# Optimization experiments

Measured on AMD Instinct MI355X. Metric: run time of the kernel, lower is better.

The kernel has to match this reference:

```python
import jax, jax.numpy as jnp
import numpy as np
from math import sqrt

EPS = 1e-5
N_BISECT = 30

def _entmax15_impl(x):
    # alpha=1.5 entmax along last axis via bisection (entmax_bisect, alpha=1.5)
    xs = x * 0.5  # (alpha-1) * x
    mx = jnp.max(xs, axis=-1, keepdims=True)
    d = xs.shape[-1]
    lo = mx - 1.0
    hi = mx - d ** -0.5  # d^{-(alpha-1)}
    def body(i, carry):
        lo, hi = carry
        mid = 0.5 * (lo + hi)
        f = jnp.sum(jnp.square(jnp.maximum(xs - mid, 0.0)), -1, keepdims=True) - 1.0
        lo = jnp.where(f > 0, mid, lo)
        hi = jnp.where(f > 0, hi, mid)
        return lo, hi
    lo, hi = jax.lax.fori_loop(0, N_BISECT, body, (lo, hi))
    tau = 0.5 * (lo + hi)
    p = jnp.square(jnp.maximum(xs - tau, 0.0))
    return p / jnp.sum(p, -1, keepdims=True)

@jax.custom_vjp
def entmax15(x):
    return _entmax15_impl(x)

def _entmax15_fwd(x):
    p = _entmax15_impl(x)
    return p, p

def _entmax15_bwd(p, g):
    # exact entmax-1.5 backward (entmax repo): gppr = sqrt(p) on support
    s = jnp.sqrt(p)
    dx = g * s
    q = jnp.sum(dx, -1, keepdims=True) / jnp.sum(s, -1, keepdims=True)
    return (dx - q * s,)

entmax15.defvjp(_entmax15_fwd, _entmax15_bwd)

def layer_norm(x, g, b):
    m = jnp.mean(x, -1, keepdims=True)
    v = jnp.var(x, -1, keepdims=True)
    return (x - m) / jnp.sqrt(v + EPS) * g + b

def mlp(x, w1, b1, w2, b2):
    return jax.nn.gelu(x @ w1 + b1, approximate=False) @ w2 + b2

def hopfield_core(q_in, k_in, H, wq, bq, wk, bk, wv, bv, wo, bo):
    # Faithful to Hopfield.forward with mix=True; `values` arg of the torch
    # module is ignored (it recomputes value_projection(key_projection(keys))).
    B, L, _ = q_in.shape
    S = k_in.shape[1]
    q = (q_in @ wq + bq).reshape(B, L, H, -1)
    k = k_in @ wk + bk
    v = (k @ wv + bv).reshape(B, S, H, -1)
    kh = k.reshape(B, S, H, -1)
    E = q.shape[-1]
    scores = jnp.einsum('blhe,bshe->bhls', q, kh) * (1.0 / sqrt(E))
    A = entmax15(scores)
    out = jnp.einsum('bhls,bshd->blhd', A, v)
    # mix=True: transpose(2,1) then view(B, L, -1) on contiguous (B,H,L,D)
    out = jnp.transpose(out, (0, 2, 1, 3)).reshape(B, L, -1)
    return out @ wo + bo

def _forward(n_heads, x, ct_wq, ct_bq, ct_wk, ct_bk, ct_wv, ct_bv, ct_wo, ct_bo,
             cs_wq, cs_bq, cs_wk, cs_bk, cs_wv, cs_bv, cs_wo, cs_bo, cs_key,
             hp_wq, hp_bq, hp_wk, hp_bk, hp_wv, hp_bv, hp_wo, hp_bo,
             n1_g, n1_b, n2_g, n2_b, n3_g, n3_b, n4_g, n4_b,
             m1_w1, m1_b1, m1_w2, m1_b2, m2_w1, m2_b1, m2_w2, m2_b2):
    b, ts_d, seg, d = x.shape
    time_in = x.reshape(b * ts_d, seg, d)
    time_enc = hopfield_core(time_in, time_in, n_heads,
                             ct_wq, ct_bq, ct_wk, ct_bk, ct_wv, ct_bv, ct_wo, ct_bo)
    dim_in = layer_norm(time_in + time_enc, n1_g, n1_b)
    dim_in = layer_norm(dim_in + mlp(dim_in, m1_w1, m1_b1, m1_w2, m1_b2), n2_g, n2_b)
    # '(b ts_d) seg d -> (b seg) ts_d d'
    series_in = dim_in.reshape(b, ts_d, seg, d).transpose(0, 2, 1, 3).reshape(b * seg, ts_d, d)
    # HopfieldPooling: learned stored patterns as keys
    pooled_keys = jnp.broadcast_to(cs_key, (b * seg,) + cs_key.shape[1:])
    series_h = hopfield_core(series_in, pooled_keys, n_heads,
                             cs_wq, cs_bq, cs_wk, cs_bk, cs_wv, cs_bv, cs_wo, cs_bo)
    pooled_h = hopfield_core(series_in, series_in, n_heads,
                             hp_wq, hp_bq, hp_wk, hp_bk, hp_wv, hp_bv, hp_wo, hp_bo)
    dim_enc = layer_norm(series_h + pooled_h, n3_g, n3_b)
    dim_enc = layer_norm(dim_enc + mlp(dim_enc, m2_w1, m2_b1, m2_w2, m2_b2), n4_g, n4_b)
    # '(b seg) ts_d d -> b ts_d seg d'
    return dim_enc.reshape(b, seg, ts_d, d).transpose(0, 2, 1, 3)

def setup_inputs() -> dict:
    b, ts_d, seg, d, h, dff, factor = 8, 32, 64, 1024, 16, 4096, 10
    keys = iter(jax.random.split(jax.random.key(0), 64))
    def rn(shape, s=0.02):
        return jax.random.normal(next(keys), shape, jnp.float32) * s
    inp = {"x": jax.random.normal(next(keys), (b, ts_d, seg, d), jnp.float32)}
    for p in ("ct", "cs", "hp"):
        inp[p + "_wq"] = rn((d, d)); inp[p + "_bq"] = rn((d,))
        inp[p + "_wk"] = rn((d, d)); inp[p + "_bk"] = rn((d,))
        inp[p + "_wv"] = rn((d, d)); inp[p + "_bv"] = rn((d,))
        inp[p + "_wo"] = rn((d, d)); inp[p + "_bo"] = rn((d,))
    inp["cs_key"] = rn((1, factor, d), 0.1)
    for i in ("1", "2", "3", "4"):
        inp["n" + i + "_g"] = jnp.ones((d,), jnp.float32)
        inp["n" + i + "_b"] = jnp.zeros((d,), jnp.float32)
    for m in ("m1", "m2"):
        inp[m + "_w1"] = rn((d, dff)); inp[m + "_b1"] = rn((dff,))
        inp[m + "_w2"] = rn((dff, d)); inp[m + "_b2"] = rn((d,))
    inp["n_heads"] = h
    return inp

def reference(x, ct_wq, ct_bq, ct_wk, ct_bk, ct_wv, ct_bv, ct_wo, ct_bo,
              cs_wq, cs_bq, cs_wk, cs_bk, cs_wv, cs_bv, cs_wo, cs_bo, cs_key,
              hp_wq, hp_bq, hp_wk, hp_bk, hp_wv, hp_bv, hp_wo, hp_bo,
              n1_g, n1_b, n2_g, n2_b, n3_g, n3_b, n4_g, n4_b,
              m1_w1, m1_b1, m1_w2, m1_b2, m2_w1, m2_b1, m2_w2, m2_b2, n_heads):
    return _forward(n_heads, x, ct_wq, ct_bq, ct_wk, ct_bk, ct_wv, ct_bv, ct_wo, ct_bo,
                    cs_wq, cs_bq, cs_wk, cs_bk, cs_wv, cs_bv, cs_wo, cs_bo, cs_key,
                    hp_wq, hp_bq, hp_wk, hp_bk, hp_wv, hp_bv, hp_wo, hp_bo,
                    n1_g, n1_b, n2_g, n2_b, n3_g, n3_b, n4_g, n4_b,
                    m1_w1, m1_b1, m1_w2, m1_b2, m2_w1, m2_b1, m2_w2, m2_b2)
```

## Files before the change

### kernel.cpp

```cpp
#include <hip/hip_runtime.h>
#include <cstdio>

typedef __bf16 bf16x8 __attribute__((ext_vector_type(8)));
typedef float f32x4 __attribute__((ext_vector_type(4)));
typedef int i32x4 __attribute__((ext_vector_type(4)));
typedef unsigned short u16x4 __attribute__((ext_vector_type(4)));

__device__ __forceinline__ float bf2f(unsigned short u) {
  union { unsigned int i; float f; } x; x.i = ((unsigned int)u) << 16; return x.f;
}
__device__ __forceinline__ unsigned short f2bf(float f) {
  union { float f; unsigned int i; } x; x.f = f;
  unsigned int r = x.i + 0x7fffu + ((x.i >> 16) & 1u);
  return (unsigned short)(r >> 16);
}

__device__ __forceinline__ void gl2lds16(const unsigned short* g, unsigned short* l) {
  __builtin_amdgcn_global_load_lds((const __attribute__((address_space(1))) unsigned int*)g,
                                   (__attribute__((address_space(3))) unsigned int*)l, 16, 0, 0);
}

__global__ __launch_bounds__(256) void k_cast(const float* __restrict__ in,
                                              unsigned short* __restrict__ out, int n4) {
  int i = blockIdx.x * 256 + threadIdx.x;
  if (i >= n4) return;
  f32x4 v = ((const f32x4*)in)[i];
  u16x4 o;
  o[0] = f2bf(v[0]); o[1] = f2bf(v[1]); o[2] = f2bf(v[2]); o[3] = f2bf(v[3]);
  ((u16x4*)out)[i] = o;
}

__global__ __launch_bounds__(256) void k_tcast(const float* __restrict__ src,
                                               unsigned short* __restrict__ dst,
                                               int K, int N) {
  __shared__ float tile[32][33];
  int gx = blockIdx.x * 32;
  int gy = blockIdx.y * 32;
  int t = threadIdx.x;
  int c = t & 31, r0 = t >> 5;
#pragma unroll
  for (int i = 0; i < 4; i++) {
    int r = r0 + i * 8;
    tile[r][c] = src[(size_t)(gy + r) * N + gx + c];
  }
  __syncthreads();
#pragma unroll
  for (int i = 0; i < 4; i++) {
    int r = r0 + i * 8;
    dst[(size_t)(gx + r) * K + gy + c] = f2bf(tile[c][r]);
  }
}

__global__ __launch_bounds__(256) void k_bfold(const float* __restrict__ bk,
                                               const float* __restrict__ wv,
                                               const float* __restrict__ bv,
                                               float* __restrict__ out) {
  int n = blockIdx.x * 256 + threadIdx.x;
  float acc = bv[n];
#pragma unroll 8
  for (int j = 0; j < 1024; j++) acc += bk[j] * wv[(size_t)j * 1024 + n];
  out[n] = acc;
}

__global__ __launch_bounds__(256) void k_cpb(const float* __restrict__ a,
                                             const float* __restrict__ b,
                                             float* __restrict__ out) {
  int t = blockIdx.x * 256 + threadIdx.x;
  out[t] = a[t];
  out[1024 + t] = b[t];
}

template <bool GELU>
__global__ __launch_bounds__(512, 2) void k_gemm8(const unsigned short* __restrict__ A,
                                                  const unsigned short* __restrict__ Bt,
                                                  const float* __restrict__ bias,
                                                  unsigned short* __restrict__ C,
                                                  int M, int N, int K) {
  __shared__ unsigned short As[2][256 * 64];
  __shared__ unsigned short Bs[2][256 * 64];
  const int rowA0 = blockIdx.y * 256, colB0 = blockIdx.x * 256;
  const int t = threadIdx.x, w = t >> 6, lane = t & 63;
  const int wm = w >> 2, wn = w & 3;
  const int g = lane >> 4, ra = lane & 15;
  const int koff0 = (((0 * 4 + g) ^ (ra & 7)) * 8);
  const int koff1 = (((1 * 4 + g) ^ (ra & 7)) * 8);
  const int srow = w * 8 + (lane >> 3);
  const int schunk = ((lane & 7) ^ ((lane >> 3) & 7)) * 8;

  f32x4 acc[8][4] = {};

  auto stageA = [&](int buf, int kk) {
#pragma unroll
    for (int gq = 0; gq < 4; gq++)
      gl2lds16(A + (size_t)(rowA0 + gq * 64 + srow) * K + kk + schunk,
               &As[buf][gq * 4096 + w * 512]);
  };
  auto stageB = [&](int buf, int kk) {
#pragma unroll
    for (int gq = 0; gq < 4; gq++)
      gl2lds16(Bt + (size_t)(colB0 + gq * 64 + srow) * K + kk + schunk,
               &Bs[buf][gq * 4096 + w * 512]);
  };

  const int NT = K >> 6;
  stageA(0, 0); stageB(0, 0);
  asm volatile("s_waitcnt vmcnt(0)" ::: "memory");
  __builtin_amdgcn_sched_barrier(0);
  __builtin_amdgcn_s_barrier();

  bf16x8 aH[4][2], bH[2][2][2];
  const int arow0 = wm * 128, brow0 = wn * 64;
  for (int j = 0; j < NT; ++j) {
    const int buf = j & 1;
    const unsigned short* Ab = &As[buf][0];
    const unsigned short* Bb = &Bs[buf][0];
#pragma unroll
    for (int fr = 0; fr < 4; fr++) {
      aH[fr][0] = *(const bf16x8*)&Ab[(arow0 + fr * 16 + ra) * 64 + koff0];
      aH[fr][1] = *(const bf16x8*)&Ab[(arow0 + fr * 16 + ra) * 64 + koff1];
    }
#pragma unroll
    for (int fc = 0; fc < 2; fc++) {
      bH[0][fc][0] = *(const bf16x8*)&Bb[(brow0 + fc * 16 + ra) * 64 + koff0];
      bH[0][fc][1] = *(const bf16x8*)&Bb[(brow0 + fc * 16 + ra) * 64 + koff1];
    }
    if (j + 1 < NT) stageA(buf ^ 1, (j + 1) << 6);
    __builtin_amdgcn_sched_barrier(0);
    __builtin_amdgcn_s_barrier();
    __builtin_amdgcn_sched_barrier(0);
    __builtin_amdgcn_s_setprio(1);
#pragma unroll
    for (int fr = 0; fr < 4; fr++)
#pragma unroll
      for (int fc = 0; fc < 2; fc++)
#pragma unroll
        for (int ks = 0; ks < 2; ks++)
          acc[fr][fc] = __builtin_amdgcn_mfma_f32_16x16x32_bf16(aH[fr][ks], bH[0][fc][ks], acc[fr][fc], 0, 0, 0);
    __builtin_amdgcn_s_setprio(0);
    __builtin_amdgcn_sched_barrier(0);
    __builtin_amdgcn_s_barrier();
#pragma unroll
    for (int fc = 0; fc < 2; fc++) {
      bH[1][fc][0] = *(const bf16x8*)&Bb[(brow0 + 32 + fc * 16 + ra) * 64 + koff0];
      bH[1][fc][1] = *(const bf16x8*)&Bb[(brow0 + 32 + fc * 16 + ra) * 64 + koff1];
    }
    if (j + 1 < NT) stageB(buf ^ 1, (j + 1) << 6);
    __builtin_amdgcn_sched_barrier(0);
    __builtin_amdgcn_s_barrier();
    __builtin_amdgcn_sched_barrier(0);
    __builtin_amdgcn_s_setprio(1);
#pragma unroll
    for (int fr = 0; fr < 4; fr++)
#pragma unroll
      for (int fc = 0; fc < 2; fc++)
#pragma unroll
        for (int ks = 0; ks < 2; ks++)
          acc[fr][2 + fc] = __builtin_amdgcn_mfma_f32_16x16x32_bf16(aH[fr][ks], bH[1][fc][ks], acc[fr][2 + fc], 0, 0, 0);
    __builtin_amdgcn_s_setprio(0);
    __builtin_amdgcn_sched_barrier(0);
    __builtin_amdgcn_s_barrier();
#pragma unroll
    for (int fr = 0; fr < 4; fr++) {
      aH[fr][0] = *(const bf16x8*)&Ab[(arow0 + 64 + fr * 16 + ra) * 64 + koff0];
      aH[fr][1] = *(const bf16x8*)&Ab[(arow0 + 64 + fr * 16 + ra) * 64 + koff1];
    }
    __builtin_amdgcn_sched_barrier(0);
    __builtin_amdgcn_s_barrier();
    __builtin_amdgcn_sched_barrier(0);
    __builtin_amdgcn_s_setprio(1);
#pragma unroll
    for (int fr = 0; fr < 4; fr++)
#pragma unroll
      for (int fc = 0; fc < 2; fc++)
#pragma unroll
        for (int ks = 0; ks < 2; ks++)
          acc[4 + fr][fc] = __builtin_amdgcn_mfma_f32_16x16x32_bf16(aH[fr][ks], bH[0][fc][ks], acc[4 + fr][fc], 0, 0, 0);
    __builtin_amdgcn_s_setprio(0);
    __builtin_amdgcn_sched_barrier(0);
    __builtin_amdgcn_s_barrier();
    __builtin_amdgcn_s_setprio(1);
#pragma unroll
    for (int fr = 0; fr < 4; fr++)
#pragma unroll
      for (int fc = 0; fc < 2; fc++)
#pragma unroll
        for (int ks = 0; ks < 2; ks++)
          acc[4 + fr][2 + fc] = __builtin_amdgcn_mfma_f32_16x16x32_bf16(aH[fr][ks], bH[1][fc][ks], acc[4 + fr][2 + fc], 0, 0, 0);
    __builtin_amdgcn_s_setprio(0);
    if (j + 1 < NT) asm volatile("s_waitcnt vmcnt(0)" ::: "memory");
    __builtin_amdgcn_sched_barrier(0);
    __builtin_amdgcn_s_barrier();
  }

  unsigned short* Ep = &As[0][0] + w * 1024;
  const int grow0 = rowA0 + wm * 128;
  const int gcol0 = colB0 + wn * 64;
  float bv[4];
#pragma unroll
  for (int n = 0; n < 4; n++) bv[n] = bias ? bias[gcol0 + n * 16 + ra] : 0.f;
  const int rdrow = lane >> 3, rg = lane & 7;
#pragma unroll
  for (int m = 0; m < 8; m++) {
#pragma unroll
    for (int n = 0; n < 4; n++)
#pragma unroll
      for (int i = 0; i < 4; i++) {
        int r = g * 4 + i;
        float v = acc[m][n][i] + bv[n];
        if (GELU) v = 0.5f * v * (1.f + erff(v * 0.70710678118654752f));
        Ep[r * 64 + ((ra + n * 16) ^ ((r & 7) << 3))] = f2bf(v);
      }
    asm volatile("s_waitcnt lgkmcnt(0)" ::: "memory");
    __builtin_amdgcn_sched_barrier(0);
#pragma unroll
    for (int p = 0; p < 2; p++) {
      int rr = p * 8 + rdrow;
      bf16x8 val = *(const bf16x8*)&Ep[rr * 64 + ((rg ^ (rr & 7)) << 3)];
      *(bf16x8*)&C[(size_t)(grow0 + m * 16 + rr) * N + gcol0 + rg * 8] = val;
    }
    asm volatile("s_waitcnt lgkmcnt(0)" ::: "memory");
  }
}

__global__ __launch_bounds__(256) void k_gemmS(const unsigned short* __restrict__ A,
                                               const unsigned short* __restrict__ Bt,
                                               const float* __restrict__ bias,
                                               unsigned short* __restrict__ C,
                                               int M, int N, int K) {
  __shared__ unsigned short As[3][128 * 32];
  __shared__ unsigned short Bs[3][128 * 32];
  const int rowA0 = blockIdx.y * 128, colB0 = blockIdx.x * 128;
  const int t = threadIdx.x, w = t >> 6, lane = t & 63;
  const int wr = w >> 1, wc = w & 1;
  const int srow = w * 16 + (lane >> 2);
  const int schunk = (lane & 3) ^ ((lane >> 3) & 3);
  const unsigned short* pa = A + (size_t)(rowA0 + srow) * K + schunk * 8;
  const unsigned short* pb = Bt + (size_t)(colB0 + srow) * K + schunk * 8;
  const size_t row64 = (size_t)64 * K;
  f32x4 acc[4][4] = {};
  const int g = lane >> 4, ra = lane & 15;
  const int gp8 = (g ^ ((ra >> 1) & 3)) * 8;
  auto stage = [&](int buf, int kk) {
    gl2lds16(pa + kk, &As[buf][w * 512]);
    gl2lds16(pa + row64 + kk, &As[buf][2048 + w * 512]);
    gl2lds16(pb + kk, &Bs[buf][w * 512]);
    gl2lds16(pb + row64 + kk, &Bs[buf][2048 + w * 512]);
  };
  const int NT = K >> 5;
  stage(0, 0);
  if (NT > 1) stage(1, 32);
  int cur = 0;
  for (int j = 0; j < NT; ++j) {
    if (j + 1 < NT) asm volatile("s_waitcnt vmcnt(4)" ::: "memory");
    else            asm volatile("s_waitcnt vmcnt(0)" ::: "memory");
    __syncthreads();
    if (j + 2 < NT) { int nb = cur + 2; if (nb >= 3) nb -= 3; stage(nb, (j + 2) * 32); }
    bf16x8 af[4], bfr[4];
#pragma unroll
    for (int m = 0; m < 4; m++)
      af[m] = *(const bf16x8*)&As[cur][(wr * 64 + m * 16 + ra) * 32 + gp8];
#pragma unroll
    for (int n = 0; n < 4; n++)
      bfr[n] = *(const bf16x8*)&Bs[cur][(wc * 64 + n * 16 + ra) * 32 + gp8];
#pragma unroll
    for (int m = 0; m < 4; m++)
#pragma unroll
      for (int n = 0; n < 4; n++)
        acc[m][n] = __builtin_amdgcn_mfma_f32_16x16x32_bf16(af[m], bfr[n], acc[m][n], 0, 0, 0);
    __syncthreads();
    cur += 1; if (cur >= 3) cur -= 3;
  }
  const int cr = g * 4, cc = ra;
#pragma unroll
  for (int m = 0; m < 4; m++) {
    int grow = rowA0 + wr * 64 + m * 16 + cr;
#pragma unroll
    for (int n = 0; n < 4; n++) {
      int gcol = colB0 + wc * 64 + n * 16 + cc;
      float bvv = bias ? bias[gcol] : 0.f;
#pragma unroll
      for (int i = 0; i < 4; i++)
        C[(size_t)(grow + i) * N + gcol] = f2bf(acc[m][n][i] + bvv);
    }
  }
}

__global__ __launch_bounds__(256) void k_gemm10(const unsigned short* __restrict__ A,
                                                const unsigned short* __restrict__ Bt,
                                                const float* __restrict__ bias,
                                                unsigned short* __restrict__ C) {
  __shared__ float af[1024];
  int m = blockIdx.x, nb = blockIdx.y;
  int t = threadIdx.x;
#pragma unroll
  for (int i = 0; i < 4; i++) af[t * 4 + i] = bf2f(A[(size_t)m * 1024 + t * 4 + i]);
  __syncthreads();
  int w = t >> 6, lane = t & 63;
  for (int n = nb * 64 + w; n < nb * 64 + 64; n += 4) {
    const unsigned short* brow = Bt + (size_t)n * 1024 + lane * 16;
    float acc = 0.f;
#pragma unroll
    for (int j = 0; j < 16; j++) acc += af[lane * 16 + j] * bf2f(brow[j]);
#pragma unroll
    for (int o = 32; o; o >>= 1) acc += __shfl_xor(acc, o);
    if (lane == 0) C[(size_t)m * 1024 + n] = f2bf(acc + bias[n]);
  }
}

template <int L, int S, bool SHARED>
__global__ __launch_bounds__(256) void k_attn(const unsigned short* __restrict__ Q,
                                              const unsigned short* __restrict__ Kb,
                                              const unsigned short* __restrict__ Vb,
                                              unsigned short* __restrict__ Out, int RS) {
  constexpr int SP = (S <= 32) ? 32 : 64;
  constexpr int QST = 72;
  constexpr int VST = SP + 8;
  constexpr int CST = SP + 4;
  __shared__ unsigned short Qs[L * QST];
  __shared__ unsigned short Ks[SP * QST];
  __shared__ unsigned short Vt[64 * VST];
  __shared__ float Sc[L * CST];
  __shared__ float Rps[L];
  const int blk = blockIdx.x, batch = blk >> 4, h = blk & 15;
  const int t = threadIdx.x, w = t >> 6, lane = t & 63;
  for (int c = t; c < L * 8; c += 256) {
    int r = c >> 3, ch = (c & 7) * 8;
    *(i32x4*)&Qs[r * QST + ch] =
        *(const i32x4*)&Q[((size_t)(batch * L + r)) * RS + h * 64 + ch];
  }
  for (int c = t; c < SP * 8; c += 256) {
    int r = c >> 3, ch = (c & 7) * 8;
    i32x4 v = {0, 0, 0, 0};
    if (r < S) {
      size_t rb = SHARED ? (size_t)r : (size_t)(batch * S + r);
      v = *(const i32x4*)&Kb[rb * RS + h * 64 + ch];
    }
    *(i32x4*)&Ks[r * QST + ch] = v;
  }
  for (int c = t; c < SP * 64; c += 256) {
    int s = c >> 6, e = c & 63;
    unsigned short v = 0;
    if (s < S) {
      size_t rb = SHARED ? (size_t)s : (size_t)(batch * S + s);
      v = Vb[rb * RS + h * 64 + e];
    }
    Vt[e * VST + s] = v;
  }
  __syncthreads();
  const int ka = (lane >> 4) * 8, ra = lane & 15;
  const int cr = (lane >> 4) * 4, cc = lane & 15;
  constexpr int NT = SP / 16, TT = (L / 16) * NT;
  for (int tt = w; tt < TT; tt += 4) {
    int m = tt / NT, n = tt % NT;
    f32x4 a = {0.f, 0.f, 0.f, 0.f};
#pragma unroll
    for (int ks = 0; ks < 2; ks++) {
      bf16x8 af = *(const bf16x8*)&Qs[(m * 16 + ra) * QST + ks * 32 + ka];
      bf16x8 bf = *(const bf16x8*)&Ks[(n * 16 + ra) * QST + ks * 32 + ka];
      a = __builtin_amdgcn_mfma_f32_16x16x32_bf16(af, bf, a, 0, 0, 0);
    }
#pragma unroll
    for (int i = 0; i < 4; i++)
      Sc[(m * 16 + cr + i) * CST + n * 16 + cc] = a[i] * 0.0625f;
  }
  __syncthreads();
  constexpr int G = 256 / L, RW = 64 / G, SL = SP / G;
  const int row = w * RW + lane / G, sub = lane % G;
  float xs[SL];
#pragma unroll
  for (int j = 0; j < SL; j++) {
    int s = sub * SL + j;
    float v = Sc[row * CST + s];
    if (S < SP && s >= S) v = -1e30f;
    xs[j] = v;
  }
  float mx = xs[0];
#pragma unroll
  for (int j = 1; j < SL; j++) mx = fmaxf(mx, xs[j]);
#pragma unroll
  for (int o = G / 2; o; o >>= 1) mx = fmaxf(mx, __shfl_xor(mx, o));
  const float hoff = (S == 64) ? 0.125f : (S == 32) ? 0.17677669529663687f : 0.31622776601683794f;
  float lo = mx - 1.f, hi = mx - hoff;
#pragma unroll 1
  for (int it = 0; it < 26; it++) {
    float mid = 0.5f * (lo + hi);
    float f = 0.f;
#pragma unroll
    for (int j = 0; j < SL; j++) { float dd = fmaxf(xs[j] - mid, 0.f); f += dd * dd; }
#pragma unroll
    for (int o = G / 2; o; o >>= 1) f += __shfl_xor(f, o);
    bool gt = f > 1.f;
    lo = gt ? mid : lo;
    hi = gt ? hi : mid;
  }
  float tau = 0.5f * (lo + hi);
  float ps = 0.f;
#pragma unroll
  for (int j = 0; j < SL; j++) { float dd = fmaxf(xs[j] - tau, 0.f); xs[j] = dd * dd; ps += xs[j]; }
#pragma unroll
  for (int o = G / 2; o; o >>= 1) ps += __shfl_xor(ps, o);
  if (sub == 0) Rps[row] = 1.f / ps;
  unsigned short* Pb = Qs;
#pragma unroll
  for (int j = 0; j < SL; j += 4) {
    u16x4 pv;
#pragma unroll
    for (int jj = 0; jj < 4; jj++) pv[jj] = f2bf(xs[j + jj]);
    *(u16x4*)&Pb[row * VST + sub * SL + j] = pv;
  }
  __syncthreads();
  constexpr int TT2 = (L / 16) * 4;
  for (int tt = w; tt < TT2; tt += 4) {
    int m = tt >> 2, n = tt & 3;
    f32x4 a = {0.f, 0.f, 0.f, 0.f};
#pragma unroll
    for (int ks = 0; ks < SP / 32; ks++) {
      bf16x8 af = *(const bf16x8*)&Pb[(m * 16 + ra) * VST + ks * 32 + ka];
      bf16x8 bf = *(const bf16x8*)&Vt[(n * 16 + ra) * VST + ks * 32 + ka];
      a = __builtin_amdgcn_mfma_f32_16x16x32_bf16(af, bf, a, 0, 0, 0);
    }
#pragma unroll
    for (int i = 0; i < 4; i++) {
      int l = m * 16 + cr + i, e = n * 16 + cc;
      float val = a[i] * Rps[l];
      int l_new = h * (L / 16) + (l >> 4);
      int cg = (l & 15) * 64 + e;
      Out[((size_t)(batch * L + l_new)) * 1024 + cg] = f2bf(val);
    }
  }
}

template <int MODE, bool F32OUT>
__global__ __launch_bounds__(256) void k_ln(const unsigned short* __restrict__ a,
                                            const unsigned short* __restrict__ b,
                                            const float* __restrict__ g,
                                            const float* __restrict__ be,
                                            void* __restrict__ outp) {
  __shared__ float red[8];
  int r = blockIdx.x, t = threadIdx.x;
  size_t base = (size_t)r * 1024 + t * 4;
  u16x4 av = *(const u16x4*)(a + base);
  u16x4 bv = *(const u16x4*)(b + base);
  float x[4];
  float s = 0.f, ss = 0.f;
#pragma unroll
  for (int i = 0; i < 4; i++) {
    x[i] = bf2f(av[i]) + bf2f(bv[i]);
    s += x[i]; ss += x[i] * x[i];
  }
#pragma unroll
  for (int o = 32; o; o >>= 1) { s += __shfl_xor(s, o); ss += __shfl_xor(ss, o); }
  int w = t >> 6;
  if ((t & 63) == 0) { red[w] = s; red[4 + w] = ss; }
  __syncthreads();
  s = red[0] + red[1] + red[2] + red[3];
  ss = red[4] + red[5] + red[6] + red[7];
  float mean = s * (1.f / 1024.f);
  float var = ss * (1.f / 1024.f) - mean * mean;
  float rstd = rsqrtf(var + 1e-5f);
  int orow;
  if (MODE == 0) orow = r;
  else if (MODE == 1) { int bi = r >> 11, rem = r & 2047; int tt = rem >> 6, sd = rem & 63; orow = (bi << 11) + sd * 32 + tt; }
  else { int bi = r >> 11, rem = r & 2047; int sd = rem >> 5, tt = rem & 31; orow = (bi << 11) + tt * 64 + sd; }
  size_t ob = (size_t)orow * 1024 + t * 4;
  if (F32OUT) {
    f32x4 y;
#pragma unroll
    for (int i = 0; i < 4; i++) y[i] = (x[i] - mean) * rstd * g[t * 4 + i] + be[t * 4 + i];
    *(f32x4*)((float*)outp + ob) = y;
  } else {
    u16x4 y;
#pragma unroll
    for (int i = 0; i < 4; i++) y[i] = f2bf((x[i] - mean) * rstd * g[t * 4 + i] + be[t * 4 + i]);
    *(u16x4*)((unsigned short*)outp + ob) = y;
  }
}


extern "C" void kernel_launch(void* const* d_in, const int* in_sizes, int n_in,
                              void* d_out, int out_size, void* d_ws, size_t ws_size,
                              hipStream_t stream) {
  const int M = 16384;
  if (n_in < 43 || in_sizes[0] != 16777216 || in_sizes[25] != 10240 || in_sizes[34] != 4194304) {
    fprintf(stderr, "kernel_launch: unexpected input layout (n_in=%d)\n", n_in);
    return;
  }
  const float* x = (const float*)d_in[0];
  const float* w[3][4]; const float* bia[3][4];
  for (int p = 0; p < 3; p++) {
    w[p][0] = (const float*)d_in[1 + 8 * p + 0]; bia[p][0] = (const float*)d_in[1 + 8 * p + 1];
    w[p][1] = (const float*)d_in[1 + 8 * p + 2]; bia[p][1] = (const float*)d_in[1 + 8 * p + 3];
    w[p][2] = (const float*)d_in[1 + 8 * p + 4]; bia[p][2] = (const float*)d_in[1 + 8 * p + 5];
    w[p][3] = (const float*)d_in[1 + 8 * p + 6]; bia[p][3] = (const float*)d_in[1 + 8 * p + 7];
  }
  const float* cs_key = (const float*)d_in[25];
  const float* ng[4]; const float* nb[4];
  for (int i = 0; i < 4; i++) { ng[i] = (const float*)d_in[26 + 2 * i]; nb[i] = (const float*)d_in[27 + 2 * i]; }
  const float* m_w1[2]; const float* m_b1[2]; const float* m_w2[2]; const float* m_b2[2];
  for (int i = 0; i < 2; i++) {
    m_w1[i] = (const float*)d_in[34 + 4 * i]; m_b1[i] = (const float*)d_in[35 + 4 * i];
    m_w2[i] = (const float*)d_in[36 + 4 * i]; m_b2[i] = (const float*)d_in[37 + 4 * i];
  }

  char* base = (char*)d_ws; size_t off = 0;
  auto alloc = [&](size_t bytes) -> void* {
    off = (off + 255) & ~(size_t)255;
    void* p = base + off; off += bytes; return p;
  };
  const size_t W1M = (size_t)1024 * 1024;
  unsigned short* W3ct = (unsigned short*)alloc(3 * W1M * 2);
  unsigned short* W3hp = (unsigned short*)alloc(3 * W1M * 2);
  unsigned short* Woct = (unsigned short*)alloc(W1M * 2);
  unsigned short* Wohp = (unsigned short*)alloc(W1M * 2);
  unsigned short* Wocs = (unsigned short*)alloc(W1M * 2);
  unsigned short* Wqcs = (unsigned short*)alloc(W1M * 2);
  unsigned short* Wkcs = (unsigned short*)alloc(W1M * 2);
  unsigned short* Wvcs = (unsigned short*)alloc(W1M * 2);
  unsigned short* Wm1u = (unsigned short*)alloc((size_t)4096 * 1024 * 2);
  unsigned short* Wm1d = (unsigned short*)alloc((size_t)1024 * 4096 * 2);
  unsigned short* Wm2u = (unsigned short*)alloc((size_t)4096 * 1024 * 2);
  unsigned short* Wm2d = (unsigned short*)alloc((size_t)1024 * 4096 * 2);
  float* b3ct = (float*)alloc(3072 * 4);
  float* b3hp = (float*)alloc(3072 * 4);
  unsigned short* KeyB = (unsigned short*)alloc((size_t)10 * 1024 * 2);
  unsigned short* Kcs = (unsigned short*)alloc((size_t)10 * 1024 * 2);
  unsigned short* Vcs = (unsigned short*)alloc((size_t)10 * 1024 * 2);
  unsigned short* S[6];
  for (int i = 0; i < 6; i++) S[i] = (unsigned short*)alloc((size_t)M * 1024 * 2);
  if (off > ws_size) {
    fprintf(stderr, "kernel_launch: ws too small: need %zu have %zu\n", off, ws_size);
    return;
  }
  unsigned short* Wvt_ct = S[1];
  unsigned short* Wraw_ct = S[1] + W1M;
  unsigned short* Wvt_hp = S[1] + 2 * W1M;
  unsigned short* Wraw_hp = S[1] + 3 * W1M;

  auto gemm = [&](const unsigned short* Ap, const unsigned short* Bt, const float* bi,
                  unsigned short* Cp, int Mm, int Nn, int Kk, bool gelu) {
    dim3 gg(Nn / 256, Mm / 256);
    if (gelu) k_gemm8<true><<<gg, 512, 0, stream>>>(Ap, Bt, bi, Cp, Mm, Nn, Kk);
    else      k_gemm8<false><<<gg, 512, 0, stream>>>(Ap, Bt, bi, Cp, Mm, Nn, Kk);
  };
  auto tc = [&](const float* src, unsigned short* dst) {
    k_tcast<<<dim3(32, 32), 256, 0, stream>>>(src, dst, 1024, 1024);
  };

  tc(w[0][0], W3ct); tc(w[0][1], W3ct + W1M);
  tc(w[2][0], W3hp); tc(w[2][1], W3hp + W1M);
  tc(w[0][3], Woct); tc(w[2][3], Wohp); tc(w[1][3], Wocs);
  tc(w[1][0], Wqcs); tc(w[1][1], Wkcs); tc(w[1][2], Wvcs);
  k_tcast<<<dim3(128, 32), 256, 0, stream>>>(m_w1[0], Wm1u, 1024, 4096);
  k_tcast<<<dim3(32, 128), 256, 0, stream>>>(m_w2[0], Wm1d, 4096, 1024);
  k_tcast<<<dim3(128, 32), 256, 0, stream>>>(m_w1[1], Wm2u, 1024, 4096);
  k_tcast<<<dim3(32, 128), 256, 0, stream>>>(m_w2[1], Wm2d, 4096, 1024);
  tc(w[0][2], Wvt_ct); k_cast<<<1024, 256, 0, stream>>>(w[0][1], Wraw_ct, 262144);
  tc(w[2][2], Wvt_hp); k_cast<<<1024, 256, 0, stream>>>(w[2][1], Wraw_hp, 262144);
  k_cast<<<16384, 256, 0, stream>>>(x, S[0], 16777216 / 4);
  k_cast<<<10, 256, 0, stream>>>(cs_key, KeyB, 10240 / 4);
  k_gemmS<<<dim3(8, 8), 256, 0, stream>>>(Wvt_ct, Wraw_ct, nullptr, W3ct + 2 * W1M, 1024, 1024, 1024);
  k_gemmS<<<dim3(8, 8), 256, 0, stream>>>(Wvt_hp, Wraw_hp, nullptr, W3hp + 2 * W1M, 1024, 1024, 1024);
  k_cpb<<<4, 256, 0, stream>>>(bia[0][0], bia[0][1], b3ct);
  k_bfold<<<4, 256, 0, stream>>>(bia[0][1], w[0][2], bia[0][2], b3ct + 2048);
  k_cpb<<<4, 256, 0, stream>>>(bia[2][0], bia[2][1], b3hp);
  k_bfold<<<4, 256, 0, stream>>>(bia[2][1], w[2][2], bia[2][2], b3hp + 2048);
  k_gemm10<<<dim3(10, 16), 256, 0, stream>>>(KeyB, Wkcs, bia[1][1], Kcs);
  k_gemm10<<<dim3(10, 16), 256, 0, stream>>>(Kcs, Wvcs, bia[1][2], Vcs);

  gemm(S[0], W3ct, b3ct, S[1], M, 3072, 1024, false);
  k_attn<64, 64, false><<<256 * 16, 256, 0, stream>>>(S[1], S[1] + 1024, S[1] + 2048, S[4], 3072);
  gemm(S[4], Woct, bia[0][3], S[5], M, 1024, 1024, false);
  k_ln<0, false><<<M, 256, 0, stream>>>(S[0], S[5], ng[0], nb[0], S[1]);
  gemm(S[1], Wm1u, m_b1[0], S[2], M, 4096, 1024, true);
  gemm(S[2], Wm1d, m_b2[0], S[0], M, 1024, 4096, false);
  k_ln<1, false><<<M, 256, 0, stream>>>(S[1], S[0], ng[1], nb[1], S[2]);

  gemm(S[2], W3hp, b3hp, S[3], M, 3072, 1024, false);
  k_attn<32, 32, false><<<512 * 16, 256, 0, stream>>>(S[3], S[3] + 1024, S[3] + 2048, S[0], 3072);
  gemm(S[0], Wohp, bia[2][3], S[1], M, 1024, 1024, false);
  gemm(S[2], Wqcs, bia[1][0], S[3], M, 1024, 1024, false);
  k_attn<32, 10, true><<<512 * 16, 256, 0, stream>>>(S[3], Kcs, Vcs, S[4], 1024);
  gemm(S[4], Wocs, bia[1][3], S[5], M, 1024, 1024, false);
  k_ln<0, false><<<M, 256, 0, stream>>>(S[5], S[1], ng[2], nb[2], S[0]);
  gemm(S[0], Wm2u, m_b1[1], S[1], M, 4096, 1024, true);
  gemm(S[1], Wm2d, m_b2[1], S[5], M, 1024, 4096, false);
  k_ln<2, true><<<M, 256, 0, stream>>>(S[0], S[5], ng[3], nb[3], d_out);
}
```

Baseline: 1.671 ms.

## Fold cross-attention query projection into keys and simplify GEMM pipeline

Precomputes Wq·K^T per head so the 10-key cross-attention scores come straight from a skinny GEMM against the normed activations. That removes the full 1024x1024 query projection. A dedicated per-row entmax kernel over 10 keys and a small PV-mix kernel replace the generic attention kernel. The main GEMM is rewritten with K-tile 32 and a simple double-buffered loop instead of the hand-scheduled 64-K pipeline, with a 128-row tile variant used for N=1024 GEMMs to raise block count. The risks are reduced precision (bf16 rounding of the folded weights), 26 bisection steps instead of 30, and losing the tuned scheduling in the big GEMMs.

```diff
diff --git a/kernel.cpp b/kernel.cpp
--- a/kernel.cpp
+++ b/kernel.cpp
@@ -70,137 +70,165 @@
   out[1024 + t] = b[t];
 }
 
-template <bool GELU>
-__global__ __launch_bounds__(512, 2) void k_gemm8(const unsigned short* __restrict__ A,
-                                                  const unsigned short* __restrict__ Bt,
-                                                  const float* __restrict__ bias,
-                                                  unsigned short* __restrict__ C,
-                                                  int M, int N, int K) {
-  __shared__ unsigned short As[2][256 * 64];
-  __shared__ unsigned short Bs[2][256 * 64];
-  const int rowA0 = blockIdx.y * 256, colB0 = blockIdx.x * 256;
+__global__ __launch_bounds__(256) void k_wqk(const unsigned short* __restrict__ wqT,
+                                             const float* __restrict__ bq,
+                                             const unsigned short* __restrict__ Kcs,
+                                             unsigned short* __restrict__ BtQK,
+                                             float* __restrict__ bqk) {
+  int n = blockIdx.x, h = n >> 4, s = n & 15, t = threadIdx.x;
+  if (s >= 10) {
+    ((u16x4*)(BtQK + (size_t)n * 1024))[t] = u16x4{0, 0, 0, 0};
+    if (t == 0) bqk[n] = 0.f;
+    return;
+  }
+  float acc[4] = {0.f, 0.f, 0.f, 0.f};
+  for (int e = 0; e < 64; e++) {
+    float kv = bf2f(Kcs[s * 1024 + h * 64 + e]);
+    u16x4 rv = ((const u16x4*)(wqT + (size_t)(h * 64 + e) * 1024))[t];
+#pragma unroll
+    for (int i = 0; i < 4; i++) acc[i] += bf2f(rv[i]) * kv;
+  }
+  u16x4 o;
+#pragma unroll
+  for (int i = 0; i < 4; i++) o[i] = f2bf(acc[i]);
+  ((u16x4*)(BtQK + (size_t)n * 1024))[t] = o;
+  if (t == 0) {
+    float b = 0.f;
+    for (int e = 0; e < 64; e++) b += bq[h * 64 + e] * bf2f(Kcs[s * 1024 + h * 64 + e]);
+    bqk[n] = b;
+  }
+}
+
+__global__ __launch_bounds__(256) void k_entmax10(const unsigned short* __restrict__ SC,
+                                                  unsigned short* __restrict__ A) {
+  int t = threadIdx.x;
+  int m = blockIdx.x * 16 + (t >> 4), h = t & 15;
+  const unsigned short* p = SC + (size_t)m * 256 + h * 16;
+  float xs[10], mx = -1e30f;
+#pragma unroll
+  for (int s = 0; s < 10; s++) { xs[s] = bf2f(p[s]) * 0.0625f; mx = fmaxf(mx, xs[s]); }
+  float lo = mx - 1.f, hi = mx - 0.31622776601683794f;
+#pragma unroll 1
+  for (int it = 0; it < 26; it++) {
+    float mid = 0.5f * (lo + hi);
+    float f = 0.f;
+#pragma unroll
+    for (int s = 0; s < 10; s++) { float dd = fmaxf(xs[s] - mid, 0.f); f += dd * dd; }
+    bool gt = f > 1.f;
+    lo = gt ? mid : lo;
+    hi = gt ? hi : mid;
+  }
+  float tau = 0.5f * (lo + hi), ps = 0.f;
+#pragma unroll
+  for (int s = 0; s < 10; s++) { float dd = fmaxf(xs[s] - tau, 0.f); xs[s] = dd * dd; ps += xs[s]; }
+  float r = 1.f / ps;
+  unsigned short* q = A + (size_t)m * 256 + h * 16;
+  u16x4 o0, o1, o2, o3;
+#pragma unroll
+  for (int i = 0; i < 4; i++) o0[i] = f2bf(xs[i] * r);
+#pragma unroll
+  for (int i = 0; i < 4; i++) o1[i] = f2bf(xs[4 + i] * r);
+  o2[0] = f2bf(xs[8] * r); o2[1] = f2bf(xs[9] * r); o2[2] = 0; o2[3] = 0;
+  o3[0] = o3[1] = o3[2] = o3[3] = 0;
+  ((u16x4*)q)[0] = o0; ((u16x4*)q)[1] = o1; ((u16x4*)q)[2] = o2; ((u16x4*)q)[3] = o3;
+}
+
+__global__ __launch_bounds__(256) void k_pvmix(const unsigned short* __restrict__ A,
+                                               const unsigned short* __restrict__ Vcs,
+                                               unsigned short* __restrict__ Out) {
+  __shared__ float Vs[10][64];
+  __shared__ float Asm[16][10];
+  const int row = blockIdx.x;
+  const int b = row >> 5, ln = row & 31;
+  const int h = ln >> 1, lbase = (ln & 1) * 16;
+  const int t = threadIdx.x;
+  if (t < 160) {
+    int j = t / 10, s = t - j * 10;
+    Asm[j][s] = bf2f(A[((size_t)(b * 32 + lbase + j)) * 256 + h * 16 + s]);
+  }
+  for (int idx = t; idx < 640; idx += 256) {
+    int s = idx >> 6, d = idx & 63;
+    Vs[s][d] = bf2f(Vcs[s * 1024 + h * 64 + d]);
+  }
+  __syncthreads();
+  const int j = t >> 4, d0 = (t & 15) * 4;
+  float acc[4] = {0.f, 0.f, 0.f, 0.f};
+#pragma unroll
+  for (int s = 0; s < 10; s++) {
+    float a = Asm[j][s];
+#pragma unroll
+    for (int i = 0; i < 4; i++) acc[i] += a * Vs[s][d0 + i];
+  }
+  u16x4 o;
+#pragma unroll
+  for (int i = 0; i < 4; i++) o[i] = f2bf(acc[i]);
+  ((u16x4*)(Out + (size_t)row * 1024))[t] = o;
+}
+
+template <int BM, bool GELU>
+__global__ __launch_bounds__(512, 4) void k_gemm(const unsigned short* __restrict__ A,
+                                                 const unsigned short* __restrict__ Bt,
+                                                 const float* __restrict__ bias,
+                                                 unsigned short* __restrict__ C,
+                                                 int M, int N, int K) {
+  constexpr int RPW = BM / 2;
+  constexpr int RF = RPW / 16;
+  __shared__ unsigned short As[2][BM * 32];
+  __shared__ unsigned short Bs[2][256 * 32];
+  const int rowA0 = blockIdx.y * BM, colB0 = blockIdx.x * 256;
   const int t = threadIdx.x, w = t >> 6, lane = t & 63;
   const int wm = w >> 2, wn = w & 3;
   const int g = lane >> 4, ra = lane & 15;
-  const int koff0 = (((0 * 4 + g) ^ (ra & 7)) * 8);
-  const int koff1 = (((1 * 4 + g) ^ (ra & 7)) * 8);
-  const int srow = w * 8 + (lane >> 3);
-  const int schunk = ((lane & 7) ^ ((lane >> 3) & 7)) * 8;
-
-  f32x4 acc[8][4] = {};
-
-  auto stageA = [&](int buf, int kk) {
-#pragma unroll
-    for (int gq = 0; gq < 4; gq++)
-      gl2lds16(A + (size_t)(rowA0 + gq * 64 + srow) * K + kk + schunk,
-               &As[buf][gq * 4096 + w * 512]);
+  const int gp8 = (g ^ ((ra >> 1) & 3)) * 8;
+  const int srow = lane >> 2;
+  const int schunk = ((lane & 3) ^ ((lane >> 3) & 3)) * 8;
+
+  f32x4 acc[RF][4] = {};
+
+  auto stage = [&](int buf, int kk) {
+#pragma unroll
+    for (int i = 0; i < BM / 128; i++)
+      gl2lds16(A + (size_t)(rowA0 + w * 16 + i * 128 + srow) * K + kk + schunk,
+               &As[buf][(w * 16 + i * 128) * 32]);
+#pragma unroll
+    for (int i = 0; i < 2; i++)
+      gl2lds16(Bt + (size_t)(colB0 + w * 16 + i * 128 + srow) * K + kk + schunk,
+               &Bs[buf][(w * 16 + i * 128) * 32]);
   };
-  auto stageB = [&](int buf, int kk) {
-#pragma unroll
-    for (int gq = 0; gq < 4; gq++)
-      gl2lds16(Bt + (size_t)(colB0 + gq * 64 + srow) * K + kk + schunk,
-               &Bs[buf][gq * 4096 + w * 512]);
-  };
-
-  const int NT = K >> 6;
-  stageA(0, 0); stageB(0, 0);
-  asm volatile("s_waitcnt vmcnt(0)" ::: "memory");
-  __builtin_amdgcn_sched_barrier(0);
-  __builtin_amdgcn_s_barrier();
-
-  bf16x8 aH[4][2], bH[2][2][2];
-  const int arow0 = wm * 128, brow0 = wn * 64;
+
+  const int NT = K >> 5;
+  stage(0, 0);
+  int buf = 0;
   for (int j = 0; j < NT; ++j) {
-    const int buf = j & 1;
+    asm volatile("s_waitcnt vmcnt(0)" ::: "memory");
+    __syncthreads();
+    if (j + 1 < NT) stage(buf ^ 1, (j + 1) * 32);
     const unsigned short* Ab = &As[buf][0];
     const unsigned short* Bb = &Bs[buf][0];
-#pragma unroll
-    for (int fr = 0; fr < 4; fr++) {
-      aH[fr][0] = *(const bf16x8*)&Ab[(arow0 + fr * 16 + ra) * 64 + koff0];
-      aH[fr][1] = *(const bf16x8*)&Ab[(arow0 + fr * 16 + ra) * 64 + koff1];
-    }
-#pragma unroll
-    for (int fc = 0; fc < 2; fc++) {
-      bH[0][fc][0] = *(const bf16x8*)&Bb[(brow0 + fc * 16 + ra) * 64 + koff0];
-      bH[0][fc][1] = *(const bf16x8*)&Bb[(brow0 + fc * 16 + ra) * 64 + koff1];
-    }
-    if (j + 1 < NT) stageA(buf ^ 1, (j + 1) << 6);
-    __builtin_amdgcn_sched_barrier(0);
-    __builtin_amdgcn_s_barrier();
-    __builtin_amdgcn_sched_barrier(0);
-    __builtin_amdgcn_s_setprio(1);
-#pragma unroll
-    for (int fr = 0; fr < 4; fr++)
-#pragma unroll
-      for (int fc = 0; fc < 2; fc++)
-#pragma unroll
-        for (int ks = 0; ks < 2; ks++)
-          acc[fr][fc] = __builtin_amdgcn_mfma_f32_16x16x32_bf16(aH[fr][ks], bH[0][fc][ks], acc[fr][fc], 0, 0, 0);
-    __builtin_amdgcn_s_setprio(0);
-    __builtin_amdgcn_sched_barrier(0);
-    __builtin_amdgcn_s_barrier();
-#pragma unroll
-    for (int fc = 0; fc < 2; fc++) {
-      bH[1][fc][0] = *(const bf16x8*)&Bb[(brow0 + 32 + fc * 16 + ra) * 64 + koff0];
-      bH[1][fc][1] = *(const bf16x8*)&Bb[(brow0 + 32 + fc * 16 + ra) * 64 + koff1];
-    }
-    if (j + 1 < NT) stageB(buf ^ 1, (j + 1) << 6);
-    __builtin_amdgcn_sched_barrier(0);
-    __builtin_amdgcn_s_barrier();
-    __builtin_amdgcn_sched_barrier(0);
-    __builtin_amdgcn_s_setprio(1);
-#pragma unroll
-    for (int fr = 0; fr < 4; fr++)
-#pragma unroll
-      for (int fc = 0; fc < 2; fc++)
-#pragma unroll
-        for (int ks = 0; ks < 2; ks++)
-          acc[fr][2 + fc] = __builtin_amdgcn_mfma_f32_16x16x32_bf16(aH[fr][ks], bH[1][fc][ks], acc[fr][2 + fc], 0, 0, 0);
-    __builtin_amdgcn_s_setprio(0);
-    __builtin_amdgcn_sched_barrier(0);
-    __builtin_amdgcn_s_barrier();
-#pragma unroll
-    for (int fr = 0; fr < 4; fr++) {
-      aH[fr][0] = *(const bf16x8*)&Ab[(arow0 + 64 + fr * 16 + ra) * 64 + koff0];
-      aH[fr][1] = *(const bf16x8*)&Ab[(arow0 + 64 + fr * 16 + ra) * 64 + koff1];
-    }
-    __builtin_amdgcn_sched_barrier(0);
-    __builtin_amdgcn_s_barrier();
-    __builtin_amdgcn_sched_barrier(0);
-    __builtin_amdgcn_s_setprio(1);
-#pragma unroll
-    for (int fr = 0; fr < 4; fr++)
-#pragma unroll
-      for (int fc = 0; fc < 2; fc++)
-#pragma unroll
-        for (int ks = 0; ks < 2; ks++)
-          acc[4 + fr][fc] = __builtin_amdgcn_mfma_f32_16x16x32_bf16(aH[fr][ks], bH[0][fc][ks], acc[4 + fr][fc], 0, 0, 0);
-    __builtin_amdgcn_s_setprio(0);
-    __builtin_amdgcn_sched_barrier(0);
-    __builtin_amdgcn_s_barrier();
-    __builtin_amdgcn_s_setprio(1);
-#pragma unroll
-    for (int fr = 0; fr < 4; fr++)
-#pragma unroll
-      for (int fc = 0; fc < 2; fc++)
-#pragma unroll
-        for (int ks = 0; ks < 2; ks++)
-          acc[4 + fr][2 + fc] = __builtin_amdgcn_mfma_f32_16x16x32_bf16(aH[fr][ks], bH[1][fc][ks], acc[4 + fr][2 + fc], 0, 0, 0);
-    __builtin_amdgcn_s_setprio(0);
-    if (j + 1 < NT) asm volatile("s_waitcnt vmcnt(0)" ::: "memory");
-    __builtin_amdgcn_sched_barrier(0);
-    __builtin_amdgcn_s_barrier();
-  }
+    bf16x8 bfr[4];
+#pragma unroll
+    for (int fc = 0; fc < 4; fc++)
+      bfr[fc] = *(const bf16x8*)&Bb[(wn * 64 + fc * 16 + ra) * 32 + gp8];
+#pragma unroll
+    for (int fr = 0; fr < RF; fr++) {
+      bf16x8 af = *(const bf16x8*)&Ab[(wm * RPW + fr * 16 + ra) * 32 + gp8];
+#pragma unroll
+      for (int fc = 0; fc < 4; fc++)
+        acc[fr][fc] = __builtin_amdgcn_mfma_f32_16x16x32_bf16(af, bfr[fc], acc[fr][fc], 0, 0, 0);
+    }
+    buf ^= 1;
+  }
+  __syncthreads();
 
   unsigned short* Ep = &As[0][0] + w * 1024;
-  const int grow0 = rowA0 + wm * 128;
+  const int grow0 = rowA0 + wm * RPW;
   const int gcol0 = colB0 + wn * 64;
   float bv[4];
 #pragma unroll
   for (int n = 0; n < 4; n++) bv[n] = bias ? bias[gcol0 + n * 16 + ra] : 0.f;
   const int rdrow = lane >> 3, rg = lane & 7;
 #pragma unroll
-  for (int m = 0; m < 8; m++) {
+  for (int m = 0; m < RF; m++) {
 #pragma unroll
     for (int n = 0; n < 4; n++)
 #pragma unroll
@@ -520,6 +548,8 @@
   unsigned short* Wm1d = (unsigned short*)alloc((size_t)1024 * 4096 * 2);
   unsigned short* Wm2u = (unsigned short*)alloc((size_t)4096 * 1024 * 2);
   unsigned short* Wm2d = (unsigned short*)alloc((size_t)1024 * 4096 * 2);
+  unsigned short* BtQK = (unsigned short*)alloc((size_t)256 * 1024 * 2);
+  float* bqk = (float*)alloc(256 * 4);
   float* b3ct = (float*)alloc(3072 * 4);
   float* b3hp = (float*)alloc(3072 * 4);
   unsigned short* KeyB = (unsigned short*)alloc((size_t)10 * 1024 * 2);
@@ -537,10 +567,16 @@
   unsigned short* Wraw_hp = S[1] + 3 * W1M;
 
   auto gemm = [&](const unsigned short* Ap, const unsigned short* Bt, const float* bi,
-                  unsigned short* Cp, int Mm, int Nn, int Kk, bool gelu) {
-    dim3 gg(Nn / 256, Mm / 256);
-    if (gelu) k_gemm8<true><<<gg, 512, 0, stream>>>(Ap, Bt, bi, Cp, Mm, Nn, Kk);
-    else      k_gemm8<false><<<gg, 512, 0, stream>>>(Ap, Bt, bi, Cp, Mm, Nn, Kk);
+                  unsigned short* Cp, int Mm, int Nn, int Kk, bool gelu, bool bm128) {
+    if (bm128) {
+      dim3 gg(Nn / 256, Mm / 128);
+      if (gelu) k_gemm<128, true><<<gg, 512, 0, stream>>>(Ap, Bt, bi, Cp, Mm, Nn, Kk);
+      else      k_gemm<128, false><<<gg, 512, 0, stream>>>(Ap, Bt, bi, Cp, Mm, Nn, Kk);
+    } else {
+      dim3 gg(Nn / 256, Mm / 256);
+      if (gelu) k_gemm<256, true><<<gg, 512, 0, stream>>>(Ap, Bt, bi, Cp, Mm, Nn, Kk);
+      else      k_gemm<256, false><<<gg, 512, 0, stream>>>(Ap, Bt, bi, Cp, Mm, Nn, Kk);
+    }
   };
   auto tc = [&](const float* src, unsigned short* dst) {
     k_tcast<<<dim3(32, 32), 256, 0, stream>>>(src, dst, 1024, 1024);
@@ -566,23 +602,25 @@
   k_bfold<<<4, 256, 0, stream>>>(bia[2][1], w[2][2], bia[2][2], b3hp + 2048);
   k_gemm10<<<dim3(10, 16), 256, 0, stream>>>(KeyB, Wkcs, bia[1][1], Kcs);
   k_gemm10<<<dim3(10, 16), 256, 0, stream>>>(Kcs, Wvcs, bia[1][2], Vcs);
-
-  gemm(S[0], W3ct, b3ct, S[1], M, 3072, 1024, false);
+  k_wqk<<<256, 256, 0, stream>>>(Wqcs, bia[1][0], Kcs, BtQK, bqk);
+
+  gemm(S[0], W3ct, b3ct, S[1], M, 3072, 1024, false, false);
   k_attn<64, 64, false><<<256 * 16, 256, 0, stream>>>(S[1], S[1] + 1024, S[1] + 2048, S[4], 3072);
-  gemm(S[4], Woct, bia[0][3], S[5], M, 1024, 1024, false);
+  gemm(S[4], Woct, bia[0][3], S[5], M, 1024, 1024, false, true);
   k_ln<0, false><<<M, 256, 0, stream>>>(S[0], S[5], ng[0], nb[0], S[1]);
-  gemm(S[1], Wm1u, m_b1[0], S[2], M, 4096, 1024, true);
-  gemm(S[2], Wm1d, m_b2[0], S[0], M, 1024, 4096, false);
+  gemm(S[1], Wm1u, m_b1[0], S[2], M, 4096, 1024, true, false);
+  gemm(S[2], Wm1d, m_b2[0], S[0], M, 1024, 4096, false, true);
   k_ln<1, false><<<M, 256, 0, stream>>>(S[1], S[0], ng[1], nb[1], S[2]);
 
-  gemm(S[2], W3hp, b3hp, S[3], M, 3072, 1024, false);
+  gemm(S[2], W3hp, b3hp, S[3], M, 3072, 1024, false, false);
   k_attn<32, 32, false><<<512 * 16, 256, 0, stream>>>(S[3], S[3] + 1024, S[3] + 2048, S[0], 3072);
-  gemm(S[0], Wohp, bia[2][3], S[1], M, 1024, 1024, false);
-  gemm(S[2], Wqcs, bia[1][0], S[3], M, 1024, 1024, false);
-  k_attn<32, 10, true><<<512 * 16, 256, 0, stream>>>(S[3], Kcs, Vcs, S[4], 1024);
-  gemm(S[4], Wocs, bia[1][3], S[5], M, 1024, 1024, false);
-  k_ln<0, false><<<M, 256, 0, stream>>>(S[5], S[1], ng[2], nb[2], S[0]);
-  gemm(S[0], Wm2u, m_b1[1], S[1], M, 4096, 1024, true);
-  gemm(S[1], Wm2d, m_b2[1], S[5], M, 1024, 4096, false);
+  gemm(S[0], Wohp, bia[2][3], S[1], M, 1024, 1024, false, true);
+  k_gemmS<<<dim3(2, 128), 256, 0, stream>>>(S[2], BtQK, bqk, S[0], M, 256, 1024);
+  k_entmax10<<<M / 16, 256, 0, stream>>>(S[0], S[0] + (size_t)M * 256);
+  k_pvmix<<<M, 256, 0, stream>>>(S[0] + (size_t)M * 256, Vcs, S[3]);
+  gemm(S[3], Wocs, bia[1][3], S[4], M, 1024, 1024, false, true);
+  k_ln<0, false><<<M, 256, 0, stream>>>(S[4], S[1], ng[2], nb[2], S[0]);
+  gemm(S[0], Wm2u, m_b1[1], S[1], M, 4096, 1024, true, false);
+  gemm(S[1], Wm2d, m_b2[1], S[5], M, 1024, 4096, false, true);
   k_ln<2, true><<<M, 256, 0, stream>>>(S[0], S[5], ng[3], nb[3], d_out);
 }
```

Result: slower. 4.329 ms (+159.1%).
